# Performance work log

Measured on AMD Instinct MI355X. Metric: run time of the kernel, lower is better.

The kernel has to match this reference:

```python
import jax, jax.numpy as jnp
import numpy as np

NUM_DRUGS, NUM_GENES = 20000, 40000
HIDDEN, HEADS, LAYERS = 128, 4, 2
D = HIDDEN // HEADS  # 32
E = 800000
BATCH = 4096


def setup_inputs() -> dict:
    key = jax.random.key(0)
    ks = jax.random.split(key, 26)
    f = lambda k, shape, s=0.05: jax.random.normal(k, shape, dtype=jnp.float32) * s
    ri = lambda k, shape, hi: jax.random.randint(k, shape, 0, hi, dtype=jnp.int32)
    inp = {
        'x_drug': f(ks[0], (NUM_DRUGS, HIDDEN), 1.0),
        'x_gene': f(ks[1], (NUM_GENES, HIDDEN), 1.0),
        # per-layer, per-node-type (0=drug, 1=gene) HGTConv linears
        'kW': f(ks[2], (LAYERS, 2, HIDDEN, HIDDEN)), 'kb': f(ks[3], (LAYERS, 2, HIDDEN)),
        'qW': f(ks[4], (LAYERS, 2, HIDDEN, HIDDEN)), 'qb': f(ks[5], (LAYERS, 2, HIDDEN)),
        'vW': f(ks[6], (LAYERS, 2, HIDDEN, HIDDEN)), 'vb': f(ks[7], (LAYERS, 2, HIDDEN)),
        'aW': f(ks[8], (LAYERS, 2, HIDDEN, HIDDEN)), 'ab': f(ks[9], (LAYERS, 2, HIDDEN)),
        'skip': f(ks[10], (LAYERS, 2), 1.0),
        # per-layer, per-edge-type (0 = drug->gene, 1 = gene->drug) relation params
        'a_rel': f(ks[11], (LAYERS, 2, HEADS, D, D)),
        'm_rel': f(ks[12], (LAYERS, 2, HEADS, D, D)),
        'p_rel': 1.0 + f(ks[13], (LAYERS, 2, HEADS), 0.1),
        # predictor MLP: Linear(256,128) -> ReLU -> Linear(128,1)
        'pW1': f(ks[14], (2 * HIDDEN, HIDDEN)), 'pb1': f(ks[15], (HIDDEN,)),
        'pW2': f(ks[16], (HIDDEN, 1)), 'pb2': f(ks[17], (1,)),
        'edge_dg_src': ri(ks[18], (E,), NUM_DRUGS),
        'edge_dg_dst': ri(ks[19], (E,), NUM_GENES),
        'edge_gd_src': ri(ks[20], (E,), NUM_GENES),
        'edge_gd_dst': ri(ks[21], (E,), NUM_DRUGS),
        'drug_idx': ri(ks[22], (BATCH,), NUM_DRUGS),
        'gene_idx': ri(ks[23], (BATCH,), NUM_GENES),  # unused by forward (per docstring)
    }
    return inp


def _rel_msg(k_src, v_src, q_dst, ar, mr, pr, src, dst, n_dst):
    # relation-specific key/value transforms: [N,H,D] x [H,D,D] -> [N,H,D]
    kr = jnp.einsum('nhd,hde->nhe', k_src, ar)
    vr = jnp.einsum('nhd,hde->nhe', v_src, mr)
    # edge-wise attention logits [E,H]
    alpha = (q_dst[dst] * kr[src]).sum(-1) * pr / np.sqrt(D)
    amax = jax.ops.segment_max(alpha, dst, num_segments=n_dst)
    a = jnp.exp(alpha - amax[dst])
    denom = jax.ops.segment_sum(a, dst, num_segments=n_dst)
    a = a / (denom[dst] + 1e-16)
    msg = vr[src] * a[:, :, None]  # [E,H,D]
    out = jax.ops.segment_sum(msg, dst, num_segments=n_dst)
    return out.reshape(n_dst, HIDDEN)


def _hgt_layer(xd, xg, kW, kb, qW, qb, vW, vb, aW, ab, skip, a_rel, m_rel, p_rel,
               dg_s, dg_d, gd_s, gd_d):
    proj = lambda x, W, b: (x @ W + b).reshape(x.shape[0], HEADS, D)
    kd, qd, vd = proj(xd, kW[0], kb[0]), proj(xd, qW[0], qb[0]), proj(xd, vW[0], vb[0])
    kg, qg, vg = proj(xg, kW[1], kb[1]), proj(xg, qW[1], qb[1]), proj(xg, vW[1], vb[1])
    # edge type 0: drug -> gene ; edge type 1: gene -> drug
    out_g = _rel_msg(kd, vd, qg, a_rel[0], m_rel[0], p_rel[0], dg_s, dg_d, NUM_GENES)
    out_d = _rel_msg(kg, vg, qd, a_rel[1], m_rel[1], p_rel[1], gd_s, gd_d, NUM_DRUGS)

    def finish(out, x, W, b, sk):
        out = jax.nn.gelu(out, approximate=False) @ W + b
        g = jax.nn.sigmoid(sk)
        return g * out + (1.0 - g) * x

    return (finish(out_d, xd, aW[0], ab[0], skip[0]),
            finish(out_g, xg, aW[1], ab[1], skip[1]))


def reference(x_drug, x_gene, kW, kb, qW, qb, vW, vb, aW, ab, skip, a_rel, m_rel, p_rel,
              pW1, pb1, pW2, pb2,
              edge_dg_src, edge_dg_dst, edge_gd_src, edge_gd_dst, drug_idx, gene_idx):
    xd, xg = x_drug, x_gene
    for l in range(LAYERS):
        xd, xg = _hgt_layer(xd, xg, kW[l], kb[l], qW[l], qb[l], vW[l], vb[l],
                            aW[l], ab[l], skip[l], a_rel[l], m_rel[l], p_rel[l],
                            edge_dg_src, edge_dg_dst, edge_gd_src, edge_gd_dst)
        xd, xg = jax.nn.relu(xd), jax.nn.relu(xg)
    drug_emb = xd[drug_idx]                                   # [B,128]
    gene_emb = jnp.broadcast_to(xg.mean(axis=0, keepdims=True),
                                (drug_idx.shape[0], HIDDEN))  # [B,128]
    comb = jnp.concatenate([drug_emb, gene_emb], axis=-1)     # [B,256]
    h = jax.nn.relu(comb @ pW1 + pb1)                         # dropout is eval no-op
    return (h @ pW2 + pb2).squeeze(-1)                        # [B]
```

## Files before the change

kernel.cpp:

```cpp
#include <hip/hip_runtime.h>
#include <hip/hip_bf16.h>
#include <math.h>

#define N_DRUG 20000
#define N_GENE 40000
#define HID 128
#define NEDGE 800000
#define NBATCH 4096

typedef unsigned short u16;
typedef unsigned int u32;
typedef __attribute__((ext_vector_type(8))) short short8;
typedef __attribute__((ext_vector_type(4))) float f32x4;

__device__ inline float gelu_exact(float x) {
    return 0.5f * x * (1.f + erff(x * 0.70710678118654752f));
}
__device__ inline u16 f2bf(float f) {
    u32 u = __float_as_uint(f);
    u += 0x7fffu + ((u >> 16) & 1u);
    return (u16)(u >> 16);
}
__device__ inline float bflo(u32 u) { return __uint_as_float(u << 16); }
__device__ inline float bfhi(u32 u) { return __uint_as_float(u & 0xffff0000u); }
__device__ inline u32 pkbf(float a, float b) { return (u32)f2bf(a) | ((u32)f2bf(b) << 16); }

#define SWZ(row, kbyte) ((row) * 256 + ((kbyte) ^ (((row) & 7) << 4)))

__global__ __launch_bounds__(256) void prologue(const float* __restrict__ kW, const float* __restrict__ kb,
                                                const float* __restrict__ qW, const float* __restrict__ qb,
                                                const float* __restrict__ vW, const float* __restrict__ vb,
                                                const float* __restrict__ a_rel, const float* __restrict__ m_rel,
                                                const float* __restrict__ p_rel,
                                                const float* __restrict__ aW, const float* __restrict__ pW1,
                                                u16* __restrict__ BFt, float* __restrict__ BB,
                                                u16* __restrict__ aWt, u16* __restrict__ W1at,
                                                int* __restrict__ cnt) {
    int b = blockIdx.x, tid = threadIdx.x;
    if (b < 768) {
        int idx = b * 256 + tid;
        int j = idx % 384;
        int k = (idx / 384) % 128;
        int lt = idx / (384 * 128);
        const float rs = 0.17677669529663687f;
        float w, bb;
        if (j < 128) {
            w = qW[(lt * 128 + k) * 128 + j];
            bb = qb[lt * 128 + j];
        } else if (j < 256) {
            int c = j - 128, h = c >> 5, e = c & 31;
            float scale = p_rel[lt * 4 + h] * rs;
            const float* ar = a_rel + ((lt * 4 + h) * 32) * 32;
            const float* kWr = kW + (lt * 128 + k) * 128 + h * 32;
            const float* kbr = kb + lt * 128 + h * 32;
            float s = 0.f, sb = 0.f;
            for (int d = 0; d < 32; d++) { float a = ar[d * 32 + e]; s += kWr[d] * a; sb += kbr[d] * a; }
            w = s * scale; bb = sb * scale;
        } else {
            int c = j - 256, h = c >> 5, e = c & 31;
            const float* mr = m_rel + ((lt * 4 + h) * 32) * 32;
            const float* vWr = vW + (lt * 128 + k) * 128 + h * 32;
            const float* vbr = vb + lt * 128 + h * 32;
            float s = 0.f, sb = 0.f;
            for (int d = 0; d < 32; d++) { float m = mr[d * 32 + e]; s += vWr[d] * m; sb += vbr[d] * m; }
            w = s; bb = sb;
        }
        BFt[((size_t)lt * 384 + j) * 128 + k] = f2bf(w);
        if (k == 0) BB[lt * 384 + j] = bb;
    } else if (b < 1024) {
        int idx = (b - 768) * 256 + tid;
        int k = idx & 127, j = (idx >> 7) & 127, lt = idx >> 14;
        aWt[idx] = f2bf(aW[((size_t)lt * 128 + k) * 128 + j]);
    } else if (b < 1088) {
        int idx = (b - 1024) * 256 + tid;
        int k = idx & 127, j = idx >> 7;
        W1at[idx] = f2bf(pW1[(size_t)k * 128 + j]);
    } else {
        int idx = (b - 1088) * 256 + tid;
        if (idx < 60000) cnt[idx] = 0;
    }
}

struct GArgs {
    const float* Af0; const float* Af1;
    const u16* Ab0;  const u16* Ab1;
    int N0; int N1; int gy0;
    const u16* Bt0;  const u16* Bt1;
    const float* bias0; const float* bias1;
    u16* QB0; u16* QB1;
    u16* KV0; u16* KV1;
    const float* skip0; const float* skip1;
    const float* Xc0; const float* Xc1;
    float* Xn0; float* Xn1;
    u16* Xb0; u16* Xb1;
    float* colPart;
    int afmt; int colTiles; int mode; int writeF32;
};

__global__ __launch_bounds__(256) void gemm_mfma(GArgs a) {
    __shared__ char As[128 * 256];
    __shared__ char Bs[64 * 256];
    __shared__ float sums[4][128];
    const int tid = threadIdx.x;
    const int set = (blockIdx.y < (unsigned)a.gy0) ? 0 : 1;
    const int by = set ? (blockIdx.y - a.gy0) : blockIdx.y;
    const int rowBase = by * 128;
    const int N = set ? a.N1 : a.N0;
    const float* Af = set ? a.Af1 : a.Af0;
    const u16* Ab = set ? a.Ab1 : a.Ab0;
    const u16* Bt = set ? a.Bt1 : a.Bt0;
    const float* bias = set ? a.bias1 : a.bias0;
    u16* QB = set ? a.QB1 : a.QB0;
    u16* KV = set ? a.KV1 : a.KV0;
    const float* skipPtr = set ? a.skip1 : a.skip0;
    const float* Xcur = set ? a.Xc1 : a.Xc0;
    float* Xn = set ? a.Xn1 : a.Xn0;
    u16* Xb = set ? a.Xb1 : a.Xb0;
    const bool doCol = (a.mode == 1) && (set == 1) && (a.colPart != nullptr);

    if (a.afmt == 0) {
#pragma unroll
        for (int it = 0; it < 16; ++it) {
            int lin = it * 256 + tid;
            int row = lin >> 5, kq = lin & 31;
            int gr = rowBase + row;
            float4 av = make_float4(0.f, 0.f, 0.f, 0.f);
            if (gr < N) av = *(const float4*)(Af + (size_t)gr * 128 + kq * 4);
            uint2 p;
            p.x = pkbf(av.x, av.y);
            p.y = pkbf(av.z, av.w);
            *(uint2*)(As + SWZ(row, kq * 8)) = p;
        }
    } else {
#pragma unroll
        for (int it = 0; it < 8; ++it) {
            int lin = it * 256 + tid;
            int row = lin >> 4, kq = lin & 15;
            int gr = rowBase + row;
            uint4 v = make_uint4(0, 0, 0, 0);
            if (gr < N) v = *(const uint4*)(Ab + (size_t)gr * 128 + kq * 8);
            *(uint4*)(As + SWZ(row, kq * 16)) = v;
        }
    }

    const int w = tid >> 6, lane = tid & 63;
    const int r15 = lane & 15;
    const int klo = (lane >> 4) << 4;
    const int cq = (lane >> 4) << 2;
    float g = 0.f;
    if (a.mode == 1) g = 1.f / (1.f + expf(-skipPtr[0]));

    for (int ct = 0; ct < a.colTiles; ++ct) {
        const int colBase = (blockIdx.x * a.colTiles + ct) * 64;
        __syncthreads();
#pragma unroll
        for (int it = 0; it < 4; ++it) {
            int lin = it * 256 + tid;
            int j = lin >> 4, kq = lin & 15;
            uint4 v = *(const uint4*)(Bt + (size_t)(colBase + j) * 128 + kq * 8);
            *(uint4*)(Bs + SWZ(j, kq * 16)) = v;
        }
        __syncthreads();

        f32x4 acc[2][4];
#pragma unroll
        for (int mt = 0; mt < 2; ++mt)
#pragma unroll
            for (int nt = 0; nt < 4; ++nt) acc[mt][nt] = (f32x4){0.f, 0.f, 0.f, 0.f};

#pragma unroll
        for (int kb = 0; kb < 4; ++kb) {
            int kbyte = kb * 64 + klo;
            short8 af[2], bf[4];
#pragma unroll
            for (int mt = 0; mt < 2; ++mt)
                af[mt] = *(short8*)(As + SWZ(w * 32 + mt * 16 + r15, kbyte));
#pragma unroll
            for (int nt = 0; nt < 4; ++nt)
                bf[nt] = *(short8*)(Bs + SWZ(nt * 16 + r15, kbyte));
#pragma unroll
            for (int mt = 0; mt < 2; ++mt)
#pragma unroll
                for (int nt = 0; nt < 4; ++nt)
                    acc[mt][nt] = __builtin_amdgcn_mfma_f32_16x16x32_bf16(bf[nt], af[mt], acc[mt][nt], 0, 0, 0);
        }

#pragma unroll
        for (int nt = 0; nt < 4; ++nt) {
            int col = colBase + nt * 16 + cq;
            float4 bi = *(const float4*)(bias + col);
            float c0 = 0.f, c1 = 0.f, c2 = 0.f, c3 = 0.f;
#pragma unroll
            for (int mt = 0; mt < 2; ++mt) {
                int grow = rowBase + w * 32 + mt * 16 + r15;
                if (grow >= N) continue;
                float v0 = acc[mt][nt][0] + bi.x;
                float v1 = acc[mt][nt][1] + bi.y;
                float v2 = acc[mt][nt][2] + bi.z;
                float v3 = acc[mt][nt][3] + bi.w;
                if (a.mode == 2) {
                    uint2 p; p.x = pkbf(v0, v1); p.y = pkbf(v2, v3);
                    if (col < 128) {
                        *(uint2*)(QB + (size_t)grow * 128 + col) = p;
                    } else if (col < 256) {
                        *(uint2*)(KV + (size_t)grow * 256 + (col - 128)) = p;
                    } else {
                        *(uint2*)(KV + (size_t)grow * 256 + 128 + (col - 256)) = p;
                    }
                } else {
                    float4 xv = *(const float4*)(Xcur + (size_t)grow * 128 + col);
                    float o0 = fmaxf(g * v0 + (1.f - g) * xv.x, 0.f);
                    float o1 = fmaxf(g * v1 + (1.f - g) * xv.y, 0.f);
                    float o2 = fmaxf(g * v2 + (1.f - g) * xv.z, 0.f);
                    float o3 = fmaxf(g * v3 + (1.f - g) * xv.w, 0.f);
                    if (a.writeF32)
                        *(float4*)(Xn + (size_t)grow * 128 + col) = make_float4(o0, o1, o2, o3);
                    if (Xb) {
                        uint2 p; p.x = pkbf(o0, o1); p.y = pkbf(o2, o3);
                        *(uint2*)(Xb + (size_t)grow * 128 + col) = p;
                    }
                    c0 += o0; c1 += o1; c2 += o2; c3 += o3;
                }
            }
            if (doCol) {
#pragma unroll
                for (int sft = 1; sft <= 8; sft <<= 1) {
                    c0 += __shfl_xor(c0, sft);
                    c1 += __shfl_xor(c1, sft);
                    c2 += __shfl_xor(c2, sft);
                    c3 += __shfl_xor(c3, sft);
                }
                if (r15 == 0) {
                    int lcol = colBase + nt * 16 + cq;
                    *(float4*)&sums[w][lcol] = make_float4(c0, c1, c2, c3);
                }
            }
        }
    }
    if (doCol) {
        __syncthreads();
        if (tid < 128) {
            float p = sums[0][tid] + sums[1][tid] + sums[2][tid] + sums[3][tid];
            a.colPart[(size_t)by * 128 + tid] = p;
        }
    }
}

__global__ __launch_bounds__(256) void fused_out_qkv(const u16* __restrict__ NUMD, const u16* __restrict__ NUMG,
                                                     const u16* __restrict__ aWt, const float* __restrict__ ab,
                                                     const float* __restrict__ skip,
                                                     const float* __restrict__ xd, const float* __restrict__ xg,
                                                     float* __restrict__ XD0, float* __restrict__ XG0,
                                                     const u16* __restrict__ BFt, const float* __restrict__ BB,
                                                     u16* __restrict__ QDB, u16* __restrict__ QGB,
                                                     u16* __restrict__ KVD, u16* __restrict__ KVG, int gy0) {
    __shared__ char As[128 * 256];
    __shared__ char Bs[64 * 256];
    const int tid = threadIdx.x;
    const int set = (blockIdx.x < (unsigned)gy0) ? 0 : 1;
    const int by = set ? (blockIdx.x - gy0) : blockIdx.x;
    const int rowBase = by * 128;
    const int N = set ? N_GENE : N_DRUG;
    const u16* A = set ? NUMG : NUMD;
    const u16* W1 = aWt + (size_t)set * 16384;
    const float* b1 = ab + (size_t)set * 128;
    const float* Xc = set ? xg : xd;
    float* Xn = set ? XG0 : XD0;
    const u16* B2 = BFt + (size_t)(2 + set) * 384 * 128;
    const float* bb2 = BB + (size_t)(2 + set) * 384;
    u16* QB = set ? QGB : QDB;
    u16* KV = set ? KVG : KVD;
    const float g = 1.f / (1.f + expf(-skip[set]));

#pragma unroll
    for (int it = 0; it < 8; ++it) {
        int lin = it * 256 + tid;
        int row = lin >> 4, kq = lin & 15;
        int gr = rowBase + row;
        uint4 v = make_uint4(0, 0, 0, 0);
        if (gr < N) v = *(const uint4*)(A + (size_t)gr * 128 + kq * 8);
        *(uint4*)(As + SWZ(row, kq * 16)) = v;
    }
    __syncthreads();

    const int w = tid >> 6, lane = tid & 63;
    const int r15 = lane & 15;
    const int klo = (lane >> 4) << 4;
    const int cq = (lane >> 4) << 2;

    f32x4 acc1[2][2][4];
#pragma unroll
    for (int ct = 0; ct < 2; ++ct) {
#pragma unroll
        for (int it = 0; it < 4; ++it) {
            int lin = it * 256 + tid;
            int j = lin >> 4, kq = lin & 15;
            uint4 v = *(const uint4*)(W1 + (size_t)(ct * 64 + j) * 128 + kq * 8);
            *(uint4*)(Bs + SWZ(j, kq * 16)) = v;
        }
        __syncthreads();
#pragma unroll
        for (int mt = 0; mt < 2; ++mt)
#pragma unroll
            for (int nt = 0; nt < 4; ++nt) acc1[ct][mt][nt] = (f32x4){0.f, 0.f, 0.f, 0.f};
#pragma unroll
        for (int kb = 0; kb < 4; ++kb) {
            int kbyte = kb * 64 + klo;
            short8 af[2], bf[4];
#pragma unroll
            for (int mt = 0; mt < 2; ++mt)
                af[mt] = *(short8*)(As + SWZ(w * 32 + mt * 16 + r15, kbyte));
#pragma unroll
            for (int nt = 0; nt < 4; ++nt)
                bf[nt] = *(short8*)(Bs + SWZ(nt * 16 + r15, kbyte));
#pragma unroll
            for (int mt = 0; mt < 2; ++mt)
#pragma unroll
                for (int nt = 0; nt < 4; ++nt)
                    acc1[ct][mt][nt] = __builtin_amdgcn_mfma_f32_16x16x32_bf16(bf[nt], af[mt], acc1[ct][mt][nt], 0, 0, 0);
        }
        __syncthreads();
    }
#pragma unroll
    for (int ct = 0; ct < 2; ++ct) {
#pragma unroll
        for (int nt = 0; nt < 4; ++nt) {
            int col = ct * 64 + nt * 16 + cq;
            float4 bi = *(const float4*)(b1 + col);
#pragma unroll
            for (int mt = 0; mt < 2; ++mt) {
                int row = w * 32 + mt * 16 + r15;
                int grow = rowBase + row;
                if (grow >= N) continue;
                float4 xv = *(const float4*)(Xc + (size_t)grow * 128 + col);
                float o0 = fmaxf(g * (acc1[ct][mt][nt][0] + bi.x) + (1.f - g) * xv.x, 0.f);
                float o1 = fmaxf(g * (acc1[ct][mt][nt][1] + bi.y) + (1.f - g) * xv.y, 0.f);
                float o2 = fmaxf(g * (acc1[ct][mt][nt][2] + bi.z) + (1.f - g) * xv.z, 0.f);
                float o3 = fmaxf(g * (acc1[ct][mt][nt][3] + bi.w) + (1.f - g) * xv.w, 0.f);
                *(float4*)(Xn + (size_t)grow * 128 + col) = make_float4(o0, o1, o2, o3);
                uint2 p; p.x = pkbf(o0, o1); p.y = pkbf(o2, o3);
                *(uint2*)(As + SWZ(row, col * 2)) = p;
            }
        }
    }

    for (int ct2 = 0; ct2 < 6; ++ct2) {
#pragma unroll
        for (int it = 0; it < 4; ++it) {
            int lin = it * 256 + tid;
            int j = lin >> 4, kq = lin & 15;
            uint4 v = *(const uint4*)(B2 + (size_t)(ct2 * 64 + j) * 128 + kq * 8);
            *(uint4*)(Bs + SWZ(j, kq * 16)) = v;
        }
        __syncthreads();
        f32x4 acc[2][4];
#pragma unroll
        for (int mt = 0; mt < 2; ++mt)
#pragma unroll
            for (int nt = 0; nt < 4; ++nt) acc[mt][nt] = (f32x4){0.f, 0.f, 0.f, 0.f};
#pragma unroll
        for (int kb = 0; kb < 4; ++kb) {
            int kbyte = kb * 64 + klo;
            short8 af[2], bf[4];
#pragma unroll
            for (int mt = 0; mt < 2; ++mt)
                af[mt] = *(short8*)(As + SWZ(w * 32 + mt * 16 + r15, kbyte));
#pragma unroll
            for (int nt = 0; nt < 4; ++nt)
                bf[nt] = *(short8*)(Bs + SWZ(nt * 16 + r15, kbyte));
#pragma unroll
            for (int mt = 0; mt < 2; ++mt)
#pragma unroll
                for (int nt = 0; nt < 4; ++nt)
                    acc[mt][nt] = __builtin_amdgcn_mfma_f32_16x16x32_bf16(bf[nt], af[mt], acc[mt][nt], 0, 0, 0);
        }
#pragma unroll
        for (int nt = 0; nt < 4; ++nt) {
            int col = ct2 * 64 + nt * 16 + cq;
            float4 bi = *(const float4*)(bb2 + col);
#pragma unroll
            for (int mt = 0; mt < 2; ++mt) {
                int grow = rowBase + w * 32 + mt * 16 + r15;
                if (grow >= N) continue;
                float v0 = acc[mt][nt][0] + bi.x;
                float v1 = acc[mt][nt][1] + bi.y;
                float v2 = acc[mt][nt][2] + bi.z;
                float v3 = acc[mt][nt][3] + bi.w;
                uint2 p; p.x = pkbf(v0, v1); p.y = pkbf(v2, v3);
                if (col < 128) {
                    *(uint2*)(QB + (size_t)grow * 128 + col) = p;
                } else if (col < 256) {
                    *(uint2*)(KV + (size_t)grow * 256 + (col - 128)) = p;
                } else {
                    *(uint2*)(KV + (size_t)grow * 256 + 128 + (col - 256)) = p;
                }
            }
        }
        __syncthreads();
    }
}

__global__ void hist2(const int* __restrict__ d0, int* __restrict__ c0,
                      const int* __restrict__ d1, int* __restrict__ c1, int gridE) {
    int b = blockIdx.x;
    const int* d; int* c; int bb;
    if (b < gridE) { d = d0; c = c0; bb = b; } else { d = d1; c = c1; bb = b - gridE; }
    int e = bb * 256 + threadIdx.x;
    if (e < NEDGE) atomicAdd(c + d[e], 1);
}

#define SCAN_NBG 10
#define SCAN_NBD 5
__global__ __launch_bounds__(256) void scan_local(const int* __restrict__ cntG,
                                                  const int* __restrict__ cntD,
                                                  int* __restrict__ outG, int* __restrict__ outD,
                                                  int* __restrict__ bsum) {
    __shared__ int tmp[256];
    int b = blockIdx.x, t = threadIdx.x;
    const int* cnt; int* out; int n; int cbase;
    if (b < SCAN_NBG) { cnt = cntG; out = outG; n = N_GENE; cbase = b * 4096; }
    else { cnt = cntD; out = outD; n = N_DRUG; cbase = (b - SCAN_NBG) * 4096; }
    int base = cbase + t * 16;
    int v[16], s = 0;
#pragma unroll
    for (int i = 0; i < 16; ++i) { int idx = base + i; v[i] = (idx < n) ? cnt[idx] : 0; s += v[i]; }
    tmp[t] = s;
    __syncthreads();
    for (int off = 1; off < 256; off <<= 1) {
        int add = (t >= off) ? tmp[t - off] : 0;
        __syncthreads();
        tmp[t] += add;
        __syncthreads();
    }
    int run = tmp[t] - s;
#pragma unroll
    for (int i = 0; i < 16; ++i) { int idx = base + i; if (idx < n) out[idx] = run; run += v[i]; }
    if (t == 255) bsum[b] = tmp[255];
}

__global__ __launch_bounds__(256) void scan_add2(int* __restrict__ outG, int* __restrict__ outD,
                                                 const int* __restrict__ bsum) {
    int b = blockIdx.x, t = threadIdx.x;
    int* out; int n; int cbase; int o = 0;
    if (b < SCAN_NBG) {
        out = outG; n = N_GENE; cbase = b * 4096;
        for (int i = 0; i < b; ++i) o += bsum[i];
    } else {
        out = outD; n = N_DRUG; cbase = (b - SCAN_NBG) * 4096;
        for (int i = SCAN_NBG; i < b; ++i) o += bsum[i];
    }
    int base = cbase + t * 16;
#pragma unroll
    for (int i = 0; i < 16; ++i) { int idx = base + i; if (idx < n) out[idx] += o; }
    if (t == 0 && b == SCAN_NBG - 1) outG[N_GENE] = NEDGE;
    if (t == 0 && b == SCAN_NBG + SCAN_NBD - 1) outD[N_DRUG] = NEDGE;
}

__global__ void scatter2(const int* __restrict__ s0, const int* __restrict__ d0,
                         const int* __restrict__ r0, int* __restrict__ cur0, int* __restrict__ o0,
                         const int* __restrict__ s1, const int* __restrict__ d1,
                         const int* __restrict__ r1, int* __restrict__ cur1, int* __restrict__ o1,
                         int gridE) {
    int b = blockIdx.x;
    const int *src, *dst, *row; int *cursor, *outp; int bb;
    if (b < gridE) { src = s0; dst = d0; row = r0; cursor = cur0; outp = o0; bb = b; }
    else { src = s1; dst = d1; row = r1; cursor = cur1; outp = o1; bb = b - gridE; }
    int e = bb * 256 + threadIdx.x;
    if (e < NEDGE) {
        int d = dst[e];
        int pos = row[d] + atomicSub(cursor + d, 1) - 1;
        outp[pos] = src[e];
    }
}

__global__ __launch_bounds__(256) void fused_attn(const int* __restrict__ rowG,
                                                  const int* __restrict__ srcG,
                                                  const u16* __restrict__ QGB,
                                                  const u16* __restrict__ KVD,
                                                  u16* __restrict__ NUMG,
                                                  const int* __restrict__ rowD,
                                                  const int* __restrict__ srcD,
                                                  const u16* __restrict__ QDB,
                                                  const u16* __restrict__ KVG,
                                                  u16* __restrict__ NUMD) {
    int node = (blockIdx.x * 256 + threadIdx.x) >> 6;
    int lane = threadIdx.x & 63;
    const int* rowStart; const int* srcSorted; const u16* Qb; const u16* KV; u16* out; int nd;
    if (node < N_GENE) { rowStart = rowG; srcSorted = srcG; Qb = QGB; KV = KVD; out = NUMG; nd = node; }
    else if (node < N_GENE + N_DRUG) { rowStart = rowD; srcSorted = srcD; Qb = QDB; KV = KVG; out = NUMD; nd = node - N_GENE; }
    else return;
    const int g = lane >> 4;
    const int sl = lane & 15;

    float qr[8];
    {
        uint4 qv = *(const uint4*)(Qb + (size_t)nd * 128 + sl * 8);
        qr[0] = bflo(qv.x); qr[1] = bfhi(qv.x);
        qr[2] = bflo(qv.y); qr[3] = bfhi(qv.y);
        qr[4] = bflo(qv.z); qr[5] = bfhi(qv.z);
        qr[6] = bflo(qv.w); qr[7] = bfhi(qv.w);
    }
    int beg = rowStart[nd], end = rowStart[nd + 1];
    float s = 0.f;
    float acc[8] = {0.f, 0.f, 0.f, 0.f, 0.f, 0.f, 0.f, 0.f};

#define FETCH(t, kk, vv)                                                \
    {                                                                   \
        int sid = __shfl(sids, 4 * (t) + g);                            \
        const u16* rowp = KV + ((size_t)sid << 8);                      \
        kk = *(const uint4*)(rowp + sl * 8);                            \
        vv = *(const uint4*)(rowp + 128 + sl * 8);                      \
    }
#define COMPUTE(t, kk, vv)                                              \
    {                                                                   \
        float part = qr[0] * bflo(kk.x) + qr[1] * bfhi(kk.x)            \
                   + qr[2] * bflo(kk.y) + qr[3] * bfhi(kk.y)            \
                   + qr[4] * bflo(kk.z) + qr[5] * bfhi(kk.z)            \
                   + qr[6] * bflo(kk.w) + qr[7] * bfhi(kk.w);           \
        part += __shfl_xor(part, 1);                                    \
        part += __shfl_xor(part, 2);                                    \
        float a = ((t) < tm) ? __expf(part) : 0.f;                      \
        s += a;                                                         \
        acc[0] += a * bflo(vv.x); acc[1] += a * bfhi(vv.x);             \
        acc[2] += a * bflo(vv.y); acc[3] += a * bfhi(vv.y);             \
        acc[4] += a * bflo(vv.z); acc[5] += a * bfhi(vv.z);             \
        acc[6] += a * bflo(vv.w); acc[7] += a * bfhi(vv.w);             \
    }

    for (int base = beg; base < end; base += 64) {
        int bn = end - base; if (bn > 64) bn = 64;
        int ld = base + lane; if (ld > end - 1) ld = end - 1;
        int sids = srcSorted[ld];
        int nIter = (bn + 3) >> 2;
        int tm = (bn - g + 3) >> 2;
        uint4 k0, v0, k1, v1;
        FETCH(0, k0, v0);
        for (int t = 0; t < nIter; t += 2) {
            if (t + 1 < nIter) FETCH(t + 1, k1, v1);
            COMPUTE(t, k0, v0);
            if (t + 1 >= nIter) break;
            if (t + 2 < nIter) FETCH(t + 2, k0, v0);
            COMPUTE(t + 1, k1, v1);
        }
    }
#undef FETCH
#undef COMPUTE

    s += __shfl_xor(s, 16);
    s += __shfl_xor(s, 32);
#pragma unroll
    for (int j = 0; j < 8; ++j) {
        acc[j] += __shfl_xor(acc[j], 16);
        acc[j] += __shfl_xor(acc[j], 32);
    }
    float inv = 1.f / (s + 1e-16f);
    float a0, a1;
    if (g == 0)      { a0 = acc[0]; a1 = acc[1]; }
    else if (g == 1) { a0 = acc[2]; a1 = acc[3]; }
    else if (g == 2) { a0 = acc[4]; a1 = acc[5]; }
    else             { a0 = acc[6]; a1 = acc[7]; }
    float r0 = gelu_exact(a0 * inv);
    float r1 = gelu_exact(a1 * inv);
    *(u32*)(out + (size_t)nd * 128 + sl * 8 + 2 * g) = pkbf(r0, r1);
}

__global__ __launch_bounds__(256) void predictor_mfma(const u16* __restrict__ Xdb,
                                                      const int* __restrict__ didx,
                                                      const u16* __restrict__ W1at,
                                                      const float* __restrict__ colPart, int nParts,
                                                      const float* __restrict__ pW1,
                                                      const float* __restrict__ pb1,
                                                      const float* __restrict__ pW2,
                                                      const float* __restrict__ pb2,
                                                      float* __restrict__ out) {
    __shared__ char As[128 * 256];
    __shared__ char Bs[128 * 256];
    __shared__ float gsL[128];
    __shared__ float c2s[128];
    const int tid = threadIdx.x;
    const int rowBase = blockIdx.x * 128;

#pragma unroll
    for (int it = 0; it < 8; ++it) {
        int lin = it * 256 + tid;
        int row = lin >> 4, kq = lin & 15;
        int dn = didx[rowBase + row];
        uint4 v = *(const uint4*)(Xdb + (size_t)dn * 128 + kq * 8);
        *(uint4*)(As + SWZ(row, kq * 16)) = v;
        uint4 wv = *(const uint4*)(W1at + (size_t)row * 128 + kq * 8);
        *(uint4*)(Bs + SWZ(row, kq * 16)) = wv;
    }
    if (tid < 128) {
        float sum = 0.f;
        for (int b = 0; b < nParts; ++b) sum += colPart[(size_t)b * 128 + tid];
        gsL[tid] = sum * (1.f / 40000.f);
    }
    __syncthreads();
    if (tid < 128) {
        float s = pb1[tid];
        for (int k = 0; k < 128; ++k) s += gsL[k] * pW1[(size_t)(128 + k) * 128 + tid];
        c2s[tid] = s;
    }
    __syncthreads();

    const int w = tid >> 6, lane = tid & 63;
    const int r15 = lane & 15;
    const int klo = (lane >> 4) << 4;
    f32x4 acc[2][8];
#pragma unroll
    for (int mt = 0; mt < 2; ++mt)
#pragma unroll
        for (int nt = 0; nt < 8; ++nt) acc[mt][nt] = (f32x4){0.f, 0.f, 0.f, 0.f};

#pragma unroll
    for (int kb = 0; kb < 4; ++kb) {
        int kbyte = kb * 64 + klo;
        short8 af[2], bf[8];
#pragma unroll
        for (int mt = 0; mt < 2; ++mt) af[mt] = *(short8*)(As + SWZ(w * 32 + mt * 16 + r15, kbyte));
#pragma unroll
        for (int nt = 0; nt < 8; ++nt) bf[nt] = *(short8*)(Bs + SWZ(nt * 16 + r15, kbyte));
#pragma unroll
        for (int mt = 0; mt < 2; ++mt)
#pragma unroll
            for (int nt = 0; nt < 8; ++nt)
                acc[mt][nt] = __builtin_amdgcn_mfma_f32_16x16x32_bf16(af[mt], bf[nt], acc[mt][nt], 0, 0, 0);
    }

    float c2v[8], w2v[8];
#pragma unroll
    for (int nt = 0; nt < 8; ++nt) {
        int col = nt * 16 + r15;
        c2v[nt] = c2s[col];
        w2v[nt] = pW2[col];
    }
    float bias2 = pb2[0];
#pragma unroll
    for (int mt = 0; mt < 2; ++mt) {
#pragma unroll
        for (int r = 0; r < 4; ++r) {
            float rsum = 0.f;
#pragma unroll
            for (int nt = 0; nt < 8; ++nt)
                rsum += fmaxf(acc[mt][nt][r] + c2v[nt], 0.f) * w2v[nt];
            rsum += __shfl_xor(rsum, 1);
            rsum += __shfl_xor(rsum, 2);
            rsum += __shfl_xor(rsum, 4);
            rsum += __shfl_xor(rsum, 8);
            if (r15 == 0)
                out[rowBase + w * 32 + mt * 16 + ((lane >> 4) << 2) + r] = rsum + bias2;
        }
    }
}

extern "C" void kernel_launch(void* const* d_in, const int* in_sizes, int n_in,
                              void* d_out, int out_size, void* d_ws, size_t ws_size,
                              hipStream_t stream) {
    const float* x_drug = (const float*)d_in[0];
    const float* x_gene = (const float*)d_in[1];
    const float* kW = (const float*)d_in[2];
    const float* kb = (const float*)d_in[3];
    const float* qW = (const float*)d_in[4];
    const float* qb = (const float*)d_in[5];
    const float* vW = (const float*)d_in[6];
    const float* vb = (const float*)d_in[7];
    const float* aW = (const float*)d_in[8];
    const float* ab = (const float*)d_in[9];
    const float* skip = (const float*)d_in[10];
    const float* a_rel = (const float*)d_in[11];
    const float* m_rel = (const float*)d_in[12];
    const float* p_rel = (const float*)d_in[13];
    const float* pW1 = (const float*)d_in[14];
    const float* pb1 = (const float*)d_in[15];
    const float* pW2 = (const float*)d_in[16];
    const float* pb2 = (const float*)d_in[17];
    const int* e_dg_s = (const int*)d_in[18];
    const int* e_dg_d = (const int*)d_in[19];
    const int* e_gd_s = (const int*)d_in[20];
    const int* e_gd_d = (const int*)d_in[21];
    const int* drug_idx = (const int*)d_in[22];

    const int gyD = (N_DRUG + 127) / 128;
    const int gyG = (N_GENE + 127) / 128;
    const int gyT = gyD + gyG;

    char* base = (char*)d_ws;
    size_t off = 0;
    auto alloc = [&](size_t bytes) { char* p = base + off; off += (bytes + 255) & ~(size_t)255; return p; };
    u16*   QDB  = (u16*)alloc((size_t)N_DRUG * 128 * 2);
    u16*   QGB  = (u16*)alloc((size_t)N_GENE * 128 * 2);
    u16*   KVD  = (u16*)alloc((size_t)N_DRUG * 256 * 2);
    u16*   KVG  = (u16*)alloc((size_t)N_GENE * 256 * 2);
    float* XD0  = (float*)alloc((size_t)N_DRUG * 128 * 4);
    float* XG0  = (float*)alloc((size_t)N_GENE * 128 * 4);
    u16*   XDb  = (u16*)alloc((size_t)N_DRUG * 128 * 2);
    u16*   NUMD = (u16*)alloc((size_t)N_DRUG * 128 * 2);
    u16*   NUMG = (u16*)alloc((size_t)N_GENE * 128 * 2);
    u16*   BFt  = (u16*)alloc((size_t)2 * 2 * 384 * 128 * 2);
    float* BB   = (float*)alloc((size_t)2 * 2 * 384 * 4);
    u16*   aWt  = (u16*)alloc((size_t)2 * 2 * 128 * 128 * 2);
    u16*   W1at = (u16*)alloc((size_t)128 * 128 * 2);
    float* colPart = (float*)alloc((size_t)gyG * 128 * 4);
    int* rowG = (int*)alloc(40001 * 4);
    int* rowD = (int*)alloc(20001 * 4);
    int* cntG = (int*)alloc(40000 * 4);
    int* cntD = (int*)alloc(20000 * 4);
    int* bsum = (int*)alloc(64 * 4);
    int* srcG = (int*)alloc((size_t)NEDGE * 4);
    int* srcD = (int*)alloc((size_t)NEDGE * 4);

    prologue<<<1323, 256, 0, stream>>>(kW, kb, qW, qb, vW, vb, a_rel, m_rel, p_rel,
                                       aW, pW1, BFt, BB, aWt, W1at, cntG);

    const int gridE = (NEDGE + 255) / 256;
    hist2<<<2 * gridE, 256, 0, stream>>>(e_dg_d, cntG, e_gd_d, cntD, gridE);
    scan_local<<<SCAN_NBG + SCAN_NBD, 256, 0, stream>>>(cntG, cntD, rowG, rowD, bsum);
    scan_add2<<<SCAN_NBG + SCAN_NBD, 256, 0, stream>>>(rowG, rowD, bsum);
    scatter2<<<2 * gridE, 256, 0, stream>>>(e_dg_s, e_dg_d, rowG, cntG, srcG,
                                            e_gd_s, e_gd_d, rowD, cntD, srcD, gridE);

    GArgs qa = {};
    qa.Af0 = x_drug; qa.Af1 = x_gene;
    qa.N0 = N_DRUG;  qa.N1 = N_GENE; qa.gy0 = gyD;
    qa.Bt0 = BFt;                    qa.Bt1 = BFt + (size_t)1 * 384 * 128;
    qa.bias0 = BB;                   qa.bias1 = BB + 384;
    qa.QB0 = QDB; qa.QB1 = QGB; qa.KV0 = KVD; qa.KV1 = KVG;
    qa.afmt = 0; qa.colTiles = 3; qa.mode = 2; qa.writeF32 = 0;
    gemm_mfma<<<dim3(2, gyT), 256, 0, stream>>>(qa);

    fused_attn<<<(N_GENE + N_DRUG + 3) / 4, 256, 0, stream>>>(
        rowG, srcG, QGB, KVD, NUMG, rowD, srcD, QDB, KVG, NUMD);

    fused_out_qkv<<<gyT, 256, 0, stream>>>(NUMD, NUMG, aWt, ab, skip, x_drug, x_gene,
                                           XD0, XG0, BFt, BB, QDB, QGB, KVD, KVG, gyD);

    fused_attn<<<(N_GENE + N_DRUG + 3) / 4, 256, 0, stream>>>(
        rowG, srcG, QGB, KVD, NUMG, rowD, srcD, QDB, KVG, NUMD);

    GArgs oa = {};
    oa.Ab0 = NUMD; oa.Ab1 = NUMG;
    oa.N0 = N_DRUG; oa.N1 = N_GENE; oa.gy0 = gyD;
    oa.Bt0 = aWt + (size_t)2 * 16384; oa.Bt1 = aWt + (size_t)3 * 16384;
    oa.bias0 = ab + 2 * 128;          oa.bias1 = ab + 3 * 128;
    oa.skip0 = skip + 2;              oa.skip1 = skip + 3;
    oa.Xc0 = XD0; oa.Xc1 = XG0;
    oa.Xb0 = XDb; oa.Xb1 = nullptr;
    oa.colPart = colPart;
    oa.afmt = 1; oa.colTiles = 2; oa.mode = 1; oa.writeF32 = 0;
    gemm_mfma<<<dim3(1, gyT), 256, 0, stream>>>(oa);

    predictor_mfma<<<NBATCH / 128, 256, 0, stream>>>(XDb, drug_idx, W1at, colPart, gyG,
                                                     pW1, pb1, pW2, pb2, (float*)d_out);
}
```

Measured before the change: 512.9 us.

## Fuse edge histogram with QKV GEMM launch and triple-buffer attention gathers

The edge-degree histogram and the first QKV projection GEMM are merged into one launch, with block index ranges dispatching to each task, so the atomic histogram overlaps with the MFMA GEMM and one kernel launch is saved. The CSR scan and scatter now run after this combined kernel. Separately, the attention edge loop moves from double-buffered to triple-buffered K/V prefetch to hide more gather latency. The cost is more registers in the attention kernel, and the combined kernel's block size, register and LDS footprint are set by the GEMM path.

```diff
diff --git a/kernel.cpp b/kernel.cpp
--- a/kernel.cpp
+++ b/kernel.cpp
@@ -97,13 +97,13 @@
     int afmt; int colTiles; int mode; int writeF32;
 };
 
-__global__ __launch_bounds__(256) void gemm_mfma(GArgs a) {
+__device__ void gemm_body(const GArgs& a, int bx, int byg) {
     __shared__ char As[128 * 256];
     __shared__ char Bs[64 * 256];
     __shared__ float sums[4][128];
     const int tid = threadIdx.x;
-    const int set = (blockIdx.y < (unsigned)a.gy0) ? 0 : 1;
-    const int by = set ? (blockIdx.y - a.gy0) : blockIdx.y;
+    const int set = (byg < a.gy0) ? 0 : 1;
+    const int by = set ? (byg - a.gy0) : byg;
     const int rowBase = by * 128;
     const int N = set ? a.N1 : a.N0;
     const float* Af = set ? a.Af1 : a.Af0;
@@ -151,7 +151,7 @@
     if (a.mode == 1) g = 1.f / (1.f + expf(-skipPtr[0]));
 
     for (int ct = 0; ct < a.colTiles; ++ct) {
-        const int colBase = (blockIdx.x * a.colTiles + ct) * 64;
+        const int colBase = (bx * a.colTiles + ct) * 64;
         __syncthreads();
 #pragma unroll
         for (int it = 0; it < 4; ++it) {
@@ -246,6 +246,26 @@
     }
 }
 
+__global__ __launch_bounds__(256) void gemm_mfma(GArgs a) {
+    gemm_body(a, blockIdx.x, blockIdx.y);
+}
+
+__global__ __launch_bounds__(256) void hist_qkv(GArgs a, int gyT,
+                                                const int* __restrict__ d0, int* __restrict__ c0,
+                                                const int* __restrict__ d1, int* __restrict__ c1,
+                                                int gridE) {
+    int b = blockIdx.x;
+    if (b < 2 * gridE) {
+        const int* d; int* c; int bb;
+        if (b < gridE) { d = d0; c = c0; bb = b; } else { d = d1; c = c1; bb = b - gridE; }
+        int e = bb * 256 + threadIdx.x;
+        if (e < NEDGE) atomicAdd(c + d[e], 1);
+    } else {
+        int r = b - 2 * gridE;
+        gemm_body(a, r / gyT, r % gyT);
+    }
+}
+
 __global__ __launch_bounds__(256) void fused_out_qkv(const u16* __restrict__ NUMD, const u16* __restrict__ NUMG,
                                                      const u16* __restrict__ aWt, const float* __restrict__ ab,
                                                      const float* __restrict__ skip,
@@ -400,15 +420,6 @@
     }
 }
 
-__global__ void hist2(const int* __restrict__ d0, int* __restrict__ c0,
-                      const int* __restrict__ d1, int* __restrict__ c1, int gridE) {
-    int b = blockIdx.x;
-    const int* d; int* c; int bb;
-    if (b < gridE) { d = d0; c = c0; bb = b; } else { d = d1; c = c1; bb = b - gridE; }
-    int e = bb * 256 + threadIdx.x;
-    if (e < NEDGE) atomicAdd(c + d[e], 1);
-}
-
 #define SCAN_NBG 10
 #define SCAN_NBD 5
 __global__ __launch_bounds__(256) void scan_local(const int* __restrict__ cntG,
@@ -533,14 +544,15 @@
         int sids = srcSorted[ld];
         int nIter = (bn + 3) >> 2;
         int tm = (bn - g + 3) >> 2;
-        uint4 k0, v0, k1, v1;
+        uint4 k0, v0, k1, v1, k2, v2;
         FETCH(0, k0, v0);
-        for (int t = 0; t < nIter; t += 2) {
-            if (t + 1 < nIter) FETCH(t + 1, k1, v1);
-            COMPUTE(t, k0, v0);
-            if (t + 1 >= nIter) break;
-            if (t + 2 < nIter) FETCH(t + 2, k0, v0);
-            COMPUTE(t + 1, k1, v1);
+        if (1 < nIter) FETCH(1, k1, v1);
+        if (2 < nIter) FETCH(2, k2, v2);
+        int t = 0;
+        for (;;) {
+            COMPUTE(t, k0, v0); { int jn = t + 3; if (jn < nIter) FETCH(jn, k0, v0); } if (++t >= nIter) break;
+            COMPUTE(t, k1, v1); { int jn = t + 3; if (jn < nIter) FETCH(jn, k1, v1); } if (++t >= nIter) break;
+            COMPUTE(t, k2, v2); { int jn = t + 3; if (jn < nIter) FETCH(jn, k2, v2); } if (++t >= nIter) break;
         }
     }
 #undef FETCH
@@ -713,11 +725,6 @@
                                        aW, pW1, BFt, BB, aWt, W1at, cntG);
 
     const int gridE = (NEDGE + 255) / 256;
-    hist2<<<2 * gridE, 256, 0, stream>>>(e_dg_d, cntG, e_gd_d, cntD, gridE);
-    scan_local<<<SCAN_NBG + SCAN_NBD, 256, 0, stream>>>(cntG, cntD, rowG, rowD, bsum);
-    scan_add2<<<SCAN_NBG + SCAN_NBD, 256, 0, stream>>>(rowG, rowD, bsum);
-    scatter2<<<2 * gridE, 256, 0, stream>>>(e_dg_s, e_dg_d, rowG, cntG, srcG,
-                                            e_gd_s, e_gd_d, rowD, cntD, srcD, gridE);
 
     GArgs qa = {};
     qa.Af0 = x_drug; qa.Af1 = x_gene;
@@ -726,7 +733,12 @@
     qa.bias0 = BB;                   qa.bias1 = BB + 384;
     qa.QB0 = QDB; qa.QB1 = QGB; qa.KV0 = KVD; qa.KV1 = KVG;
     qa.afmt = 0; qa.colTiles = 3; qa.mode = 2; qa.writeF32 = 0;
-    gemm_mfma<<<dim3(2, gyT), 256, 0, stream>>>(qa);
+    hist_qkv<<<2 * gridE + 2 * gyT, 256, 0, stream>>>(qa, gyT, e_dg_d, cntG, e_gd_d, cntD, gridE);
+
+    scan_local<<<SCAN_NBG + SCAN_NBD, 256, 0, stream>>>(cntG, cntD, rowG, rowD, bsum);
+    scan_add2<<<SCAN_NBG + SCAN_NBD, 256, 0, stream>>>(rowG, rowD, bsum);
+    scatter2<<<2 * gridE, 256, 0, stream>>>(e_dg_s, e_dg_d, rowG, cntG, srcG,
+                                            e_gd_s, e_gd_d, rowD, cntD, srcD, gridE);
 
     fused_attn<<<(N_GENE + N_DRUG + 3) / 4, 256, 0, stream>>>(
         rowG, srcG, QGB, KVD, NUMG, rowD, srcD, QDB, KVG, NUMD);
```

Measured after the change: 521.4 us. About the same (+1.7%).
